# Performance work log

Hardware: AMD Instinct MI355X
Metric: run time of the kernel (lower is better)

## Reference

```python
import jax, jax.numpy as jnp
import numpy as np

EMB = 1024
HEADS = 16
HD = EMB // HEADS
EPS = 1e-5

def _ln(x, g, b):
    m = jnp.mean(x, axis=-1, keepdims=True)
    v = jnp.mean((x - m) ** 2, axis=-1, keepdims=True)
    return (x - m) * jax.lax.rsqrt(v + EPS) * g + b

def setup_inputs() -> dict:
    key = jax.random.key(0)
    ks = jax.random.split(key, 12)
    s_in = 1.0 / np.sqrt(EMB)
    s_ff = 1.0 / np.sqrt(4 * EMB)
    return {
        "x": jax.random.normal(ks[0], (2, 2048, EMB), jnp.float32),
        "wq": jax.random.uniform(ks[1], (HEADS, EMB, HD), jnp.float32, -s_in, s_in),
        "wk": jax.random.uniform(ks[2], (HEADS, EMB, HD), jnp.float32, -s_in, s_in),
        "wv": jax.random.uniform(ks[3], (HEADS, EMB, HD), jnp.float32, -s_in, s_in),
        "wo": jax.random.uniform(ks[4], (EMB, EMB), jnp.float32, -s_in, s_in),
        "bo": jax.random.uniform(ks[5], (EMB,), jnp.float32, -s_in, s_in),
        "g1": jnp.ones((EMB,), jnp.float32),
        "b1": jnp.zeros((EMB,), jnp.float32),
        "g2": jnp.ones((EMB,), jnp.float32),
        "b2": jnp.zeros((EMB,), jnp.float32),
        "w1": jax.random.uniform(ks[6], (EMB, 4 * EMB), jnp.float32, -s_in, s_in),
        "bf1": jax.random.uniform(ks[7], (4 * EMB,), jnp.float32, -s_in, s_in),
        "w2": jax.random.uniform(ks[8], (4 * EMB, EMB), jnp.float32, -s_ff, s_ff),
        "bf2": jax.random.uniform(ks[9], (EMB,), jnp.float32, -s_ff, s_ff),
    }

def reference(x, wq, wk, wv, wo, bo, g1, b1, g2, b2, w1, bf1, w2, bf2):
    B, T, C = x.shape
    h = _ln(x, g1, b1)
    # all heads batched: [B,H,T,HD]
    q = jnp.einsum('btc,hcd->bhtd', h, wq)
    k = jnp.einsum('btc,hcd->bhtd', h, wk)
    v = jnp.einsum('btc,hcd->bhtd', h, wv)
    # NOTE: original scales by full emb_size C**-0.5, not head_size
    scores = jnp.einsum('bhtd,bhsd->bhts', q, k) * (C ** -0.5)
    causal = jnp.tril(jnp.ones((T, T), bool))
    scores = jnp.where(causal, scores, -jnp.inf)
    w = jax.nn.softmax(scores, axis=-1)
    attn = jnp.einsum('bhts,bhsd->bhtd', w, v)
    attn = attn.transpose(0, 2, 1, 3).reshape(B, T, C)  # concat heads
    x = x + attn @ wo + bo
    h2 = _ln(x, g2, b2)
    ffn = jax.nn.relu(h2 @ w1 + bf1) @ w2 + bf2
    return x + ffn
```

## Files before the change

### kernel.cpp

```cpp
#include <hip/hip_runtime.h>
#include <hip/hip_bf16.h>

typedef __bf16 bf16x8 __attribute__((ext_vector_type(8)));
typedef float f32x4 __attribute__((ext_vector_type(4)));
typedef short s16x8 __attribute__((ext_vector_type(8)));

#define DEV __device__ __forceinline__

DEV float b2f(unsigned short u) {
  unsigned int x = ((unsigned int)u) << 16;
  return __builtin_bit_cast(float, x);
}
DEV unsigned short f2b(float f) {
  unsigned int x = __builtin_bit_cast(unsigned int, f);
  x += 0x7fffu + ((x >> 16) & 1u);
  return (unsigned short)(x >> 16);
}
DEV unsigned int f2b2(float a, float b) {
  float2 t; t.x = a; t.y = b;
  __hip_bfloat162 v = __float22bfloat162_rn(t);
  unsigned int r;
  __builtin_memcpy(&r, &v, 4);
  return r;
}
DEV f32x4 mfma16(bf16x8 a, bf16x8 b, f32x4 c) {
  return __builtin_amdgcn_mfma_f32_16x16x32_bf16(a, b, c, 0, 0, 0);
}
DEV void gl2lds16(const unsigned short* g, unsigned short* l) {
  __builtin_amdgcn_global_load_lds(
      (const __attribute__((address_space(1))) void*)g,
      (__attribute__((address_space(3))) void*)l, 16, 0, 0);
}

__global__ __launch_bounds__(256)
void transpose_k(const float* __restrict__ in, unsigned short* __restrict__ out,
                 int K, int N, long zin, long zout) {
  __shared__ float tile[32][33];
  in  += (size_t)blockIdx.z * zin;
  out += (size_t)blockIdx.z * zout;
  int n0 = blockIdx.x * 32, k0 = blockIdx.y * 32;
  int tx = threadIdx.x, ty = threadIdx.y;
  #pragma unroll
  for (int i = ty; i < 32; i += 8)
    tile[i][tx] = in[(size_t)(k0 + i) * N + n0 + tx];
  __syncthreads();
  #pragma unroll
  for (int i = ty; i < 32; i += 8)
    out[(size_t)(n0 + i) * K + k0 + tx] = f2b(tile[tx][i]);
}

__global__ __launch_bounds__(256)
void transpose_qkv(const float* __restrict__ wq, const float* __restrict__ wk,
                   const float* __restrict__ wv, unsigned short* __restrict__ out) {
  __shared__ float tile[32][33];
  const int z = blockIdx.z;
  const float* in = (z < 16) ? (wq + (size_t)z * 65536)
                  : (z < 32) ? (wk + (size_t)(z - 16) * 65536)
                             : (wv + (size_t)(z - 32) * 65536);
  unsigned short* o = out + (size_t)z * 65536;
  int n0 = blockIdx.x * 32, k0 = blockIdx.y * 32;
  int tx = threadIdx.x, ty = threadIdx.y;
  #pragma unroll
  for (int i = ty; i < 32; i += 8)
    tile[i][tx] = in[(size_t)(k0 + i) * 64 + n0 + tx];
  __syncthreads();
  #pragma unroll
  for (int i = ty; i < 32; i += 8)
    o[(size_t)(n0 + i) * 1024 + k0 + tx] = f2b(tile[tx][i]);
}

__global__ __launch_bounds__(256)
void ln_kernel(const float* __restrict__ x, const float* __restrict__ g,
               const float* __restrict__ b, unsigned short* __restrict__ o) {
  __shared__ float rs[4];
  __shared__ float rq[4];
  int row = blockIdx.x, tid = threadIdx.x;
  const float* xr = x + (size_t)row * 1024;
  float4 raw = ((const float4*)xr)[tid];
  float s = raw.x + raw.y + raw.z + raw.w;
  float q = raw.x*raw.x + raw.y*raw.y + raw.z*raw.z + raw.w*raw.w;
  #pragma unroll
  for (int off = 32; off > 0; off >>= 1) {
    s += __shfl_down(s, off);
    q += __shfl_down(q, off);
  }
  int wave = tid >> 6;
  if ((tid & 63) == 0) { rs[wave] = s; rq[wave] = q; }
  __syncthreads();
  float ts = rs[0] + rs[1] + rs[2] + rs[3];
  float tq = rq[0] + rq[1] + rq[2] + rq[3];
  float mean = ts * (1.0f/1024.0f);
  float var = tq * (1.0f/1024.0f) - mean*mean;
  float rstd = rsqrtf(var + 1e-5f);
  float4 gr = ((const float4*)g)[tid];
  float4 br = ((const float4*)b)[tid];
  float o0 = (raw.x-mean)*rstd*gr.x + br.x;
  float o1 = (raw.y-mean)*rstd*gr.y + br.y;
  float o2 = (raw.z-mean)*rstd*gr.z + br.z;
  float o3 = (raw.w-mean)*rstd*gr.w + br.w;
  uint2 ov;
  ov.x = f2b2(o0, o1);
  ov.y = f2b2(o2, o3);
  ((uint2*)(o + (size_t)row * 1024))[tid] = ov;
}

template<bool RELU, bool BIAS, bool VFUSE>
__global__ __launch_bounds__(512, 2)
void gemm8p(const unsigned short* __restrict__ A, const unsigned short* __restrict__ Bt,
            const float* __restrict__ bias, void* __restrict__ Cv,
            unsigned short* __restrict__ vT, int NTn, int N, int K) {
  __shared__ unsigned short As[4][256*32];
  __shared__ unsigned short Bs[4][256*32];
  const int tid = threadIdx.x;
  const int lane = tid & 63, wave = tid >> 6;
  const int quad = lane >> 4, l16 = lane & 15;
  const int wm = wave >> 2, wn = wave & 3;
  const int nwg = gridDim.x;
  const int id = blockIdx.x;
  const int id2 = (id & 7) * (nwg >> 3) + (id >> 3);
  const int mt = id2 / NTn, nt = id2 % NTn;
  const int m0 = mt * 256, n0 = nt * 256;

  f32x4 acc[8][4];
  #pragma unroll
  for (int i = 0; i < 8; ++i)
    #pragma unroll
    for (int j = 0; j < 4; ++j) acc[i][j] = (f32x4){0.f, 0.f, 0.f, 0.f};

  const int srow = tid >> 2;
  const int scc  = (((tid & 3) ^ ((srow >> 1) & 3)) * 8);
  const unsigned short* Ab = A + (size_t)m0 * K;
  const unsigned short* Bb = Bt + (size_t)n0 * K;

  const int NT = K >> 5;
  const int H  = NT << 2;

  auto stage = [&](int h) {
    const int Tt = h >> 2, part = h & 3, kk = Tt << 5;
    const int buf = Tt & 3;
    if (part == 0)
      gl2lds16(Ab + (size_t)srow * K + kk + scc,         &As[buf][tid * 8]);
    else if (part == 1)
      gl2lds16(Ab + (size_t)(srow + 128) * K + kk + scc, &As[buf][4096 + tid * 8]);
    else if (part == 2)
      gl2lds16(Bb + (size_t)srow * K + kk + scc,         &Bs[buf][tid * 8]);
    else
      gl2lds16(Bb + (size_t)(srow + 128) * K + kk + scc, &Bs[buf][4096 + tid * 8]);
  };

  #pragma unroll
  for (int h = 0; h < 10; ++h) stage(h);
  asm volatile("s_waitcnt vmcnt(6)" ::: "memory");
  asm volatile("s_barrier" ::: "memory");

  const int qsw = (quad ^ ((l16 >> 1) & 3)) * 8;
  const int arow0 = wm * 128 + l16;
  const int brow0 = wn * 64 + l16;

  for (int T = 0; T < NT; ++T) {
    const int buf = T & 3;
    bf16x8 bq[4];
    {
      bf16x8 af[4];
      #pragma unroll
      for (int i = 0; i < 4; ++i)
        af[i] = __builtin_bit_cast(bf16x8,
          *(const s16x8*)&As[buf][(arow0 + i*16)*32 + qsw]);
      #pragma unroll
      for (int j = 0; j < 4; ++j)
        bq[j] = __builtin_bit_cast(bf16x8,
          *(const s16x8*)&Bs[buf][(brow0 + j*16)*32 + qsw]);
      const int h = 4*T + 10;
      if (h < H)     stage(h);
      if (h + 1 < H) stage(h + 1);
      asm volatile("s_barrier" ::: "memory");
      __builtin_amdgcn_s_setprio(1);
      #pragma unroll
      for (int i = 0; i < 4; ++i)
        #pragma unroll
        for (int j = 0; j < 4; ++j)
          acc[i][j] = mfma16(af[i], bq[j], acc[i][j]);
      __builtin_amdgcn_s_setprio(0);
      asm volatile("s_barrier" ::: "memory");
    }
    {
      bf16x8 af[4];
      #pragma unroll
      for (int i = 0; i < 4; ++i)
        af[i] = __builtin_bit_cast(bf16x8,
          *(const s16x8*)&As[buf][(arow0 + 64 + i*16)*32 + qsw]);
      const int h = 4*T + 12;
      if (h < H)     stage(h);
      if (h + 1 < H) stage(h + 1);
      if (T + 3 < NT)      { asm volatile("s_waitcnt vmcnt(6)" ::: "memory"); }
      else if (T + 2 < NT) { asm volatile("s_waitcnt vmcnt(4)" ::: "memory"); }
      else if (T + 1 < NT) { asm volatile("s_waitcnt vmcnt(0)" ::: "memory"); }
      asm volatile("s_barrier" ::: "memory");
      __builtin_amdgcn_s_setprio(1);
      #pragma unroll
      for (int i = 0; i < 4; ++i)
        #pragma unroll
        for (int j = 0; j < 4; ++j)
          acc[4 + i][j] = mfma16(af[i], bq[j], acc[4 + i][j]);
      __builtin_amdgcn_s_setprio(0);
      asm volatile("s_barrier" ::: "memory");
    }
  }

  #pragma unroll
  for (int ii = 0; ii < 8; ++ii) {
    const int row = m0 + wm*128 + ii*16 + quad*4;
    #pragma unroll
    for (int j = 0; j < 4; ++j) {
      const int col = n0 + wn*64 + j*16 + l16;
      if (VFUSE && col >= 2048) {
        const int b = row >> 11, tloc = row & 2047;
        const int h = (col - 2048) >> 6, d = col & 63;
        ushort4 pk;
        pk.x = f2b(acc[ii][j][0]);
        pk.y = f2b(acc[ii][j][1]);
        pk.z = f2b(acc[ii][j][2]);
        pk.w = f2b(acc[ii][j][3]);
        *(ushort4*)&vT[((size_t)((b*16 + h)*64 + d))*2048 + tloc] = pk;
      } else {
        float bv = BIAS ? bias[col] : 0.f;
        #pragma unroll
        for (int r = 0; r < 4; ++r) {
          float v = acc[ii][j][r] + bv;
          if (RELU) v = fmaxf(v, 0.f);
          ((unsigned short*)Cv)[(size_t)(row + r) * N + col] = f2b(v);
        }
      }
    }
  }
}

__global__ __launch_bounds__(512)
void gemm_t128(const unsigned short* __restrict__ A, const unsigned short* __restrict__ Bt,
               const float* __restrict__ bias, const float* __restrict__ resid,
               float* __restrict__ C, int M, int N, int K) {
  __shared__ unsigned short SMEM[6*128*64];
  const int tid = threadIdx.x;
  const int lane = tid & 63;
  const int quad = lane >> 4, l16 = lane & 15;
  const int wave = tid >> 6;
  const int sub = wave >> 2;
  const int wq = wave & 3;
  const int wm = (wq >> 1) * 64, wn = (wq & 1) * 64;
  const int id = blockIdx.x;
  const int xcd = id & 7, i2 = id >> 3;
  const int mt = (xcd << 2) | (i2 >> 3);
  const int nt = i2 & 7;
  const int m0 = mt * 128, n0 = nt * 128;

  f32x4 acc[4][4];
  #pragma unroll
  for (int i = 0; i < 4; ++i)
    #pragma unroll
    for (int j = 0; j < 4; ++j) acc[i][j] = (f32x4){0.f, 0.f, 0.f, 0.f};

  const int srow = tid >> 3;
  const int scc  = ((tid & 7) ^ (srow & 7)) * 8;
  const unsigned short* Ab = A + (size_t)m0 * K;
  const unsigned short* Bb = Bt + (size_t)n0 * K;

  auto stage = [&](int buf, int k0) {
    unsigned short* Ad = SMEM + buf * 8192;
    unsigned short* Bd = SMEM + 24576 + buf * 8192;
    gl2lds16(Ab + (size_t)srow * K + k0 + scc,        Ad + tid * 8);
    gl2lds16(Ab + (size_t)(srow + 64) * K + k0 + scc, Ad + 4096 + tid * 8);
    gl2lds16(Bb + (size_t)srow * K + k0 + scc,        Bd + tid * 8);
    gl2lds16(Bb + (size_t)(srow + 64) * K + k0 + scc, Bd + 4096 + tid * 8);
  };

  const int niter = K >> 6;
  stage(0, 0);
  stage(1, 64);

  const int cc = sub * 4 + quad;
  int bufc = 0;
  for (int it = 0; it < niter; ++it) {
    if (it + 1 < niter) {
      asm volatile("s_waitcnt vmcnt(4)" ::: "memory");
    } else {
      asm volatile("s_waitcnt vmcnt(0)" ::: "memory");
    }
    __builtin_amdgcn_s_barrier();
    if (it + 2 < niter) {
      int bufn = bufc + 2; if (bufn >= 3) bufn -= 3;
      stage(bufn, (it + 2) * 64);
    }
    const unsigned short* Ar = SMEM + bufc * 8192;
    const unsigned short* Br = SMEM + 24576 + bufc * 8192;
    bf16x8 af[4], bfr[4];
    #pragma unroll
    for (int i = 0; i < 4; ++i) {
      const int R = wm + i*16 + l16;
      af[i] = __builtin_bit_cast(bf16x8,
        *(const s16x8*)&Ar[R*64 + ((cc ^ (R & 7)) * 8)]);
    }
    #pragma unroll
    for (int j = 0; j < 4; ++j) {
      const int R = wn + j*16 + l16;
      bfr[j] = __builtin_bit_cast(bf16x8,
        *(const s16x8*)&Br[R*64 + ((cc ^ (R & 7)) * 8)]);
    }
    #pragma unroll
    for (int i = 0; i < 4; ++i)
      #pragma unroll
      for (int j = 0; j < 4; ++j)
        acc[i][j] = mfma16(af[i], bfr[j], acc[i][j]);
    bufc = (bufc == 2) ? 0 : bufc + 1;
  }

  __syncthreads();
  float* ex = (float*)&SMEM[0];
  float* w = ex + wq * 4096;
  if (sub == 1) {
    #pragma unroll
    for (int i = 0; i < 4; ++i)
      #pragma unroll
      for (int j = 0; j < 4; ++j)
        *(f32x4*)&w[(i*4 + j)*256 + lane*4] = acc[i][j];
  }
  __syncthreads();
  if (sub == 1) return;

  #pragma unroll
  for (int i = 0; i < 4; ++i) {
    const int row = m0 + wm + i*16 + quad*4;
    #pragma unroll
    for (int j = 0; j < 4; ++j) {
      f32x4 oth = *(const f32x4*)&w[(i*4 + j)*256 + lane*4];
      const int col = n0 + wn + j*16 + l16;
      const float bv = bias[col];
      #pragma unroll
      for (int r = 0; r < 4; ++r)
        C[(size_t)(row + r) * N + col] =
            acc[i][j][r] + oth[r] + bv + resid[(size_t)(row + r) * N + col];
    }
  }
}

__global__ __launch_bounds__(256)
void attn_kernel(const unsigned short* __restrict__ qkv,
                 const unsigned short* __restrict__ vT,
                 unsigned short* __restrict__ outc) {
  __shared__ unsigned short Ks[2][64*64];
  __shared__ unsigned short Vs[2][64*64];
  __shared__ unsigned short Ps[4*16*72];
  const int tid = threadIdx.x, lane = tid & 63, wave = tid >> 6;
  const int quad = lane >> 4, l16 = lane & 15;
  const int bh = blockIdx.y, b = bh >> 4, h = bh & 15;
  const int jA = blockIdx.x, jB = 31 - jA;
  const size_t tokbase = (size_t)b * 2048 * 3072;
  const unsigned short* Q  = qkv + tokbase + h * 64;
  const unsigned short* Kg = qkv + tokbase + 1024 + h * 64;
  const unsigned short* Vg = vT + (size_t)bh * 64 * 2048;

  const s16x8 ones_s = {0x3F80, 0x3F80, 0x3F80, 0x3F80, 0x3F80, 0x3F80, 0x3F80, 0x3F80};
  const bf16x8 onesf = __builtin_bit_cast(bf16x8, ones_s);

  bf16x8 qf[2][2];
  #pragma unroll
  for (int t = 0; t < 2; ++t) {
    const int qrow = (t ? jB : jA) * 64 + wave * 16 + l16;
    #pragma unroll
    for (int s = 0; s < 2; ++s) {
      s16x8 raw = *(const s16x8*)(Q + (size_t)qrow * 3072 + s * 32 + quad * 8);
      unsigned short* rp = (unsigned short*)&raw;
      #pragma unroll
      for (int j = 0; j < 8; ++j) rp[j] = f2b(b2f(rp[j]) * 0.03125f);
      qf[t][s] = __builtin_bit_cast(bf16x8, raw);
    }
  }

  f32x4 accO[2][4];
  f32x4 accS[2] = {(f32x4){0.f,0.f,0.f,0.f}, (f32x4){0.f,0.f,0.f,0.f}};
  #pragma unroll
  for (int t = 0; t < 2; ++t)
    #pragma unroll
    for (int i = 0; i < 4; ++i) accO[t][i] = (f32x4){0.f, 0.f, 0.f, 0.f};

  const int r8 = lane >> 3;
  const int cs = (((lane & 7) ^ r8) * 8);

  auto stage = [&](int buf, int kv0) {
    #pragma unroll
    for (int i = 0; i < 2; ++i) {
      int row = wave * 16 + i * 8;
      gl2lds16(Kg + (size_t)(kv0 + row + r8) * 3072 + cs, &Ks[buf][row * 64 + lane * 8]);
      gl2lds16(Vg + (size_t)(row + r8) * 2048 + kv0 + cs, &Vs[buf][row * 64 + lane * 8]);
    }
  };

  const int ntile = jB + 1;
  stage(0, 0);
  __syncthreads();

  for (int it = 0; it < ntile; ++it) {
    const int buf = it & 1;
    if (it + 1 < ntile) stage(buf ^ 1, (it + 1) * 64);

    #pragma unroll
    for (int t = 0; t < 2; ++t) {
      const int jT = t ? jB : jA;
      if (it > jT) continue;
      f32x4 sv[4];
      #pragma unroll
      for (int ni = 0; ni < 4; ++ni) {
        sv[ni] = (f32x4){0.f, 0.f, 0.f, 0.f};
        #pragma unroll
        for (int s = 0; s < 2; ++s) {
          bf16x8 kf = __builtin_bit_cast(bf16x8,
            *(const s16x8*)&Ks[buf][(ni*16 + l16)*64 + (((s*4 + quad) ^ (l16 & 7)) * 8)]);
          sv[ni] = mfma16(qf[t][s], kf, sv[ni]);
        }
      }
      if (it == jT) {
        const int rowg = jT*64 + wave*16 + quad*4;
        const int kv0 = it * 64;
        #pragma unroll
        for (int ni = 0; ni < 4; ++ni) {
          const int colg = kv0 + ni*16 + l16;
          #pragma unroll
          for (int r = 0; r < 4; ++r)
            if (colg > rowg + r) sv[ni][r] = -__builtin_inff();
        }
      }
      #pragma unroll
      for (int ni = 0; ni < 4; ++ni) {
        float p0 = __expf(sv[ni][0]);
        float p1 = __expf(sv[ni][1]);
        float p2 = __expf(sv[ni][2]);
        float p3 = __expf(sv[ni][3]);
        unsigned int u01 = f2b2(p0, p1);
        unsigned int u23 = f2b2(p2, p3);
        const int base = wave*1152 + ni*16 + l16;
        Ps[base + (quad*4 + 0)*72] = (unsigned short)u01;
        Ps[base + (quad*4 + 1)*72] = (unsigned short)(u01 >> 16);
        Ps[base + (quad*4 + 2)*72] = (unsigned short)u23;
        Ps[base + (quad*4 + 3)*72] = (unsigned short)(u23 >> 16);
      }
      __asm__ volatile("s_waitcnt lgkmcnt(0)" ::: "memory");
      #pragma unroll
      for (int s = 0; s < 2; ++s) {
        bf16x8 pf = __builtin_bit_cast(bf16x8,
          *(const s16x8*)&Ps[wave*1152 + l16*72 + s*32 + quad*8]);
        accS[t] = mfma16(pf, onesf, accS[t]);
        #pragma unroll
        for (int ni = 0; ni < 4; ++ni) {
          bf16x8 vf = __builtin_bit_cast(bf16x8,
            *(const s16x8*)&Vs[buf][(ni*16 + l16)*64 + (((s*4 + quad) ^ (l16 & 7)) * 8)]);
          accO[t][ni] = mfma16(pf, vf, accO[t][ni]);
        }
      }
    }
    __syncthreads();
  }

  #pragma unroll
  for (int t = 0; t < 2; ++t) {
    const int rowg = (t ? jB : jA)*64 + wave*16 + quad*4;
    float inv[4];
    #pragma unroll
    for (int r = 0; r < 4; ++r) inv[r] = __builtin_amdgcn_rcpf(accS[t][r]);
    #pragma unroll
    for (int ni = 0; ni < 4; ++ni)
      #pragma unroll
      for (int r = 0; r < 4; ++r)
        outc[(size_t)(b*2048 + rowg + r) * 1024 + h*64 + ni*16 + l16]
          = f2b(accO[t][ni][r] * inv[r]);
  }
}

extern "C" void kernel_launch(void* const* d_in, const int* in_sizes, int n_in,
                              void* d_out, int out_size, void* d_ws, size_t ws_size,
                              hipStream_t stream) {
  (void)in_sizes; (void)n_in; (void)out_size; (void)ws_size;
  const float* x   = (const float*)d_in[0];
  const float* wq  = (const float*)d_in[1];
  const float* wk  = (const float*)d_in[2];
  const float* wv  = (const float*)d_in[3];
  const float* wo  = (const float*)d_in[4];
  const float* bo  = (const float*)d_in[5];
  const float* g1  = (const float*)d_in[6];
  const float* b1  = (const float*)d_in[7];
  const float* g2  = (const float*)d_in[8];
  const float* b2  = (const float*)d_in[9];
  const float* w1  = (const float*)d_in[10];
  const float* bf1 = (const float*)d_in[11];
  const float* w2  = (const float*)d_in[12];
  const float* bf2 = (const float*)d_in[13];
  float* out = (float*)d_out;

  unsigned short* ws    = (unsigned short*)d_ws;
  unsigned short* wqkvt = ws;
  unsigned short* wot   = wqkvt + 3*1024*1024;
  unsigned short* w1t   = wot   + 1024*1024;
  unsigned short* w2t   = w1t   + 4096*1024;
  unsigned short* hbuf  = w2t   + 4096*1024;
  unsigned short* qkvb  = hbuf  + 4096*1024;
  unsigned short* attnb = qkvb  + (size_t)4096*3072;
  float*          x2b   = (float*)(attnb + 4096*1024);
  unsigned short* vTb   = (unsigned short*)x2b;
  unsigned short* midb  = qkvb;

  dim3 tb(32, 8);
  transpose_qkv<<<dim3(2,32,48), tb, 0, stream>>>(wq, wk, wv, wqkvt);
  transpose_k<<<dim3(32,32,1),  tb, 0, stream>>>(wo, wot, 1024, 1024, 0, 0);
  transpose_k<<<dim3(128,32,1), tb, 0, stream>>>(w1, w1t, 1024, 4096, 0, 0);
  transpose_k<<<dim3(32,128,1), tb, 0, stream>>>(w2, w2t, 4096, 1024, 0, 0);

  ln_kernel<<<4096, 256, 0, stream>>>(x, g1, b1, hbuf);
  gemm8p<false,false,true><<<192, 512, 0, stream>>>(
      hbuf, wqkvt, nullptr, qkvb, vTb, 12, 3072, 1024);
  attn_kernel<<<dim3(16,32), 256, 0, stream>>>(qkvb, vTb, attnb);
  gemm_t128<<<256, 512, 0, stream>>>(attnb, wot, bo, x, x2b, 4096, 1024, 1024);
  ln_kernel<<<4096, 256, 0, stream>>>(x2b, g2, b2, hbuf);
  gemm8p<true,true,false><<<256, 512, 0, stream>>>(
      hbuf, w1t, bf1, midb, nullptr, 16, 4096, 1024);
  gemm_t128<<<256, 512, 0, stream>>>(midb, w2t, bf2, x2b, out, 4096, 1024, 4096);
}
```

Before: 325.8 us.

## Split paired causal attention blocks into one query tile per block with XCD-aware mapping

Each attention block previously handled two query tiles (j and 31-j) so causal work was balanced per block and shared K/V staging. Now each block handles a single 64-row query tile, doubling the grid to 1024 blocks, and the 1D block id is remapped so that all blocks for a given batch-head land on the same XCD, improving L2 reuse of K/V. This trades away the built-in load balance and the shared K/V loads for more parallelism and cache locality, so blocks now have very uneven work (1 to 32 tiles).

```diff
diff --git a/kernel.cpp b/kernel.cpp
--- a/kernel.cpp
+++ b/kernel.cpp
@@ -351,8 +351,12 @@
   __shared__ unsigned short Ps[4*16*72];
   const int tid = threadIdx.x, lane = tid & 63, wave = tid >> 6;
   const int quad = lane >> 4, l16 = lane & 15;
-  const int bh = blockIdx.y, b = bh >> 4, h = bh & 15;
-  const int jA = blockIdx.x, jB = 31 - jA;
+  const int id = blockIdx.x;
+  const int xcd = id & 7;
+  const int w = id >> 3;
+  const int bh = xcd * 4 + (w & 3);
+  const int j = w >> 2;
+  const int b = bh >> 4, h = bh & 15;
   const size_t tokbase = (size_t)b * 2048 * 3072;
   const unsigned short* Q  = qkv + tokbase + h * 64;
   const unsigned short* Kg = qkv + tokbase + 1024 + h * 64;
@@ -361,26 +365,23 @@
   const s16x8 ones_s = {0x3F80, 0x3F80, 0x3F80, 0x3F80, 0x3F80, 0x3F80, 0x3F80, 0x3F80};
   const bf16x8 onesf = __builtin_bit_cast(bf16x8, ones_s);
 
-  bf16x8 qf[2][2];
-  #pragma unroll
-  for (int t = 0; t < 2; ++t) {
-    const int qrow = (t ? jB : jA) * 64 + wave * 16 + l16;
+  bf16x8 qf[2];
+  {
+    const int qrow = j * 64 + wave * 16 + l16;
     #pragma unroll
     for (int s = 0; s < 2; ++s) {
       s16x8 raw = *(const s16x8*)(Q + (size_t)qrow * 3072 + s * 32 + quad * 8);
       unsigned short* rp = (unsigned short*)&raw;
       #pragma unroll
-      for (int j = 0; j < 8; ++j) rp[j] = f2b(b2f(rp[j]) * 0.03125f);
-      qf[t][s] = __builtin_bit_cast(bf16x8, raw);
-    }
-  }
-
-  f32x4 accO[2][4];
-  f32x4 accS[2] = {(f32x4){0.f,0.f,0.f,0.f}, (f32x4){0.f,0.f,0.f,0.f}};
-  #pragma unroll
-  for (int t = 0; t < 2; ++t)
-    #pragma unroll
-    for (int i = 0; i < 4; ++i) accO[t][i] = (f32x4){0.f, 0.f, 0.f, 0.f};
+      for (int k = 0; k < 8; ++k) rp[k] = f2b(b2f(rp[k]) * 0.03125f);
+      qf[s] = __builtin_bit_cast(bf16x8, raw);
+    }
+  }
+
+  f32x4 accO[4];
+  f32x4 accS = (f32x4){0.f, 0.f, 0.f, 0.f};
+  #pragma unroll
+  for (int i = 0; i < 4; ++i) accO[i] = (f32x4){0.f, 0.f, 0.f, 0.f};
 
   const int r8 = lane >> 3;
   const int cs = (((lane & 7) ^ r8) * 8);
@@ -394,7 +395,7 @@
     }
   };
 
-  const int ntile = jB + 1;
+  const int ntile = j + 1;
   stage(0, 0);
   __syncthreads();
 
@@ -402,76 +403,68 @@
     const int buf = it & 1;
     if (it + 1 < ntile) stage(buf ^ 1, (it + 1) * 64);
 
-    #pragma unroll
-    for (int t = 0; t < 2; ++t) {
-      const int jT = t ? jB : jA;
-      if (it > jT) continue;
-      f32x4 sv[4];
+    f32x4 sv[4];
+    #pragma unroll
+    for (int ni = 0; ni < 4; ++ni) {
+      sv[ni] = (f32x4){0.f, 0.f, 0.f, 0.f};
+      #pragma unroll
+      for (int s = 0; s < 2; ++s) {
+        bf16x8 kf = __builtin_bit_cast(bf16x8,
+          *(const s16x8*)&Ks[buf][(ni*16 + l16)*64 + (((s*4 + quad) ^ (l16 & 7)) * 8)]);
+        sv[ni] = mfma16(qf[s], kf, sv[ni]);
+      }
+    }
+    if (it == j) {
+      const int rowg = j*64 + wave*16 + quad*4;
+      const int kv0 = it * 64;
       #pragma unroll
       for (int ni = 0; ni < 4; ++ni) {
-        sv[ni] = (f32x4){0.f, 0.f, 0.f, 0.f};
+        const int colg = kv0 + ni*16 + l16;
         #pragma unroll
-        for (int s = 0; s < 2; ++s) {
-          bf16x8 kf = __builtin_bit_cast(bf16x8,
-            *(const s16x8*)&Ks[buf][(ni*16 + l16)*64 + (((s*4 + quad) ^ (l16 & 7)) * 8)]);
-          sv[ni] = mfma16(qf[t][s], kf, sv[ni]);
-        }
+        for (int r = 0; r < 4; ++r)
+          if (colg > rowg + r) sv[ni][r] = -__builtin_inff();
       }
-      if (it == jT) {
-        const int rowg = jT*64 + wave*16 + quad*4;
-        const int kv0 = it * 64;
-        #pragma unroll
-        for (int ni = 0; ni < 4; ++ni) {
-          const int colg = kv0 + ni*16 + l16;
-          #pragma unroll
-          for (int r = 0; r < 4; ++r)
-            if (colg > rowg + r) sv[ni][r] = -__builtin_inff();
-        }
+    }
+    #pragma unroll
+    for (int ni = 0; ni < 4; ++ni) {
+      float p0 = __expf(sv[ni][0]);
+      float p1 = __expf(sv[ni][1]);
+      float p2 = __expf(sv[ni][2]);
+      float p3 = __expf(sv[ni][3]);
+      unsigned int u01 = f2b2(p0, p1);
+      unsigned int u23 = f2b2(p2, p3);
+      const int base = wave*1152 + ni*16 + l16;
+      Ps[base + (quad*4 + 0)*72] = (unsigned short)u01;
+      Ps[base + (quad*4 + 1)*72] = (unsigned short)(u01 >> 16);
+      Ps[base + (quad*4 + 2)*72] = (unsigned short)u23;
+      Ps[base + (quad*4 + 3)*72] = (unsigned short)(u23 >> 16);
+    }
+    __asm__ volatile("s_waitcnt lgkmcnt(0)" ::: "memory");
+    #pragma unroll
+    for (int s = 0; s < 2; ++s) {
+      bf16x8 pf = __builtin_bit_cast(bf16x8,
+        *(const s16x8*)&Ps[wave*1152 + l16*72 + s*32 + quad*8]);
+      accS = mfma16(pf, onesf, accS);
+      #pragma unroll
+      for (int ni = 0; ni < 4; ++ni) {
+        bf16x8 vf = __builtin_bit_cast(bf16x8,
+          *(const s16x8*)&Vs[buf][(ni*16 + l16)*64 + (((s*4 + quad) ^ (l16 & 7)) * 8)]);
+        accO[ni] = mfma16(pf, vf, accO[ni]);
       }
-      #pragma unroll
-      for (int ni = 0; ni < 4; ++ni) {
-        float p0 = __expf(sv[ni][0]);
-        float p1 = __expf(sv[ni][1]);
-        float p2 = __expf(sv[ni][2]);
-        float p3 = __expf(sv[ni][3]);
-        unsigned int u01 = f2b2(p0, p1);
-        unsigned int u23 = f2b2(p2, p3);
-        const int base = wave*1152 + ni*16 + l16;
-        Ps[base + (quad*4 + 0)*72] = (unsigned short)u01;
-        Ps[base + (quad*4 + 1)*72] = (unsigned short)(u01 >> 16);
-        Ps[base + (quad*4 + 2)*72] = (unsigned short)u23;
-        Ps[base + (quad*4 + 3)*72] = (unsigned short)(u23 >> 16);
-      }
-      __asm__ volatile("s_waitcnt lgkmcnt(0)" ::: "memory");
-      #pragma unroll
-      for (int s = 0; s < 2; ++s) {
-        bf16x8 pf = __builtin_bit_cast(bf16x8,
-          *(const s16x8*)&Ps[wave*1152 + l16*72 + s*32 + quad*8]);
-        accS[t] = mfma16(pf, onesf, accS[t]);
-        #pragma unroll
-        for (int ni = 0; ni < 4; ++ni) {
-          bf16x8 vf = __builtin_bit_cast(bf16x8,
-            *(const s16x8*)&Vs[buf][(ni*16 + l16)*64 + (((s*4 + quad) ^ (l16 & 7)) * 8)]);
-          accO[t][ni] = mfma16(pf, vf, accO[t][ni]);
-        }
-      }
     }
     __syncthreads();
   }
 
-  #pragma unroll
-  for (int t = 0; t < 2; ++t) {
-    const int rowg = (t ? jB : jA)*64 + wave*16 + quad*4;
-    float inv[4];
-    #pragma unroll
-    for (int r = 0; r < 4; ++r) inv[r] = __builtin_amdgcn_rcpf(accS[t][r]);
-    #pragma unroll
-    for (int ni = 0; ni < 4; ++ni)
-      #pragma unroll
-      for (int r = 0; r < 4; ++r)
-        outc[(size_t)(b*2048 + rowg + r) * 1024 + h*64 + ni*16 + l16]
-          = f2b(accO[t][ni][r] * inv[r]);
-  }
+  const int rowg = j*64 + wave*16 + quad*4;
+  float inv[4];
+  #pragma unroll
+  for (int r = 0; r < 4; ++r) inv[r] = __builtin_amdgcn_rcpf(accS[r]);
+  #pragma unroll
+  for (int ni = 0; ni < 4; ++ni)
+    #pragma unroll
+    for (int r = 0; r < 4; ++r)
+      outc[(size_t)(b*2048 + rowg + r) * 1024 + h*64 + ni*16 + l16]
+        = f2b(accO[ni][r] * inv[r]);
 }
 
 extern "C" void kernel_launch(void* const* d_in, const int* in_sizes, int n_in,
@@ -515,7 +508,7 @@
   ln_kernel<<<4096, 256, 0, stream>>>(x, g1, b1, hbuf);
   gemm8p<false,false,true><<<192, 512, 0, stream>>>(
       hbuf, wqkvt, nullptr, qkvb, vTb, 12, 3072, 1024);
-  attn_kernel<<<dim3(16,32), 256, 0, stream>>>(qkvb, vTb, attnb);
+  attn_kernel<<<1024, 256, 0, stream>>>(qkvb, vTb, attnb);
   gemm_t128<<<256, 512, 0, stream>>>(attnb, wot, bo, x, x2b, 4096, 1024, 1024);
   ln_kernel<<<4096, 256, 0, stream>>>(x2b, g2, b2, hbuf);
   gemm8p<true,true,false><<<256, 512, 0, stream>>>(
```

After: 325.9 us. Within noise of the previous version (+0.0%).

## Transpose score MFMA for vectorized P stores, use exp2, and remap attention blocks per XCD

Applied to the files above, without the earlier changes.

The attention kernel now computes S^T by swapping the MFMA operands, so each lane holds four consecutive kv scores for one query row. That lets the bf16 probabilities go to shared memory as a single 8-byte store instead of four scattered 2-byte stores. The softmax scale is folded with log2(e) so exp2f replaces __expf. The grid is flattened to 1D and remapped so the four heads sharing an XCD (id&7) reuse K/V in that XCD's L2. The causal mask indexing is rewritten to match the transposed layout, and the remapping assumes round-robin dispatch of blocks across the 8 XCDs.

```diff
diff --git a/kernel.cpp b/kernel.cpp
--- a/kernel.cpp
+++ b/kernel.cpp
@@ -351,8 +351,11 @@
   __shared__ unsigned short Ps[4*16*72];
   const int tid = threadIdx.x, lane = tid & 63, wave = tid >> 6;
   const int quad = lane >> 4, l16 = lane & 15;
-  const int bh = blockIdx.y, b = bh >> 4, h = bh & 15;
-  const int jA = blockIdx.x, jB = 31 - jA;
+  const int id = blockIdx.x;
+  const int xcd = id & 7;
+  const int bh = xcd * 4 + ((id >> 3) & 3);
+  const int jA = id >> 5, jB = 31 - jA;
+  const int b = bh >> 4, h = bh & 15;
   const size_t tokbase = (size_t)b * 2048 * 3072;
   const unsigned short* Q  = qkv + tokbase + h * 64;
   const unsigned short* Kg = qkv + tokbase + 1024 + h * 64;
@@ -370,7 +373,7 @@
       s16x8 raw = *(const s16x8*)(Q + (size_t)qrow * 3072 + s * 32 + quad * 8);
       unsigned short* rp = (unsigned short*)&raw;
       #pragma unroll
-      for (int j = 0; j < 8; ++j) rp[j] = f2b(b2f(rp[j]) * 0.03125f);
+      for (int k = 0; k < 8; ++k) rp[k] = f2b(b2f(rp[k]) * 0.0450842305f);
       qf[t][s] = __builtin_bit_cast(bf16x8, raw);
     }
   }
@@ -414,33 +417,29 @@
         for (int s = 0; s < 2; ++s) {
           bf16x8 kf = __builtin_bit_cast(bf16x8,
             *(const s16x8*)&Ks[buf][(ni*16 + l16)*64 + (((s*4 + quad) ^ (l16 & 7)) * 8)]);
-          sv[ni] = mfma16(qf[t][s], kf, sv[ni]);
+          sv[ni] = mfma16(kf, qf[t][s], sv[ni]);
         }
       }
       if (it == jT) {
-        const int rowg = jT*64 + wave*16 + quad*4;
-        const int kv0 = it * 64;
+        const int qr = jT*64 + wave*16 + l16;
+        const int kvb = it*64 + quad*4;
         #pragma unroll
         for (int ni = 0; ni < 4; ++ni) {
-          const int colg = kv0 + ni*16 + l16;
           #pragma unroll
           for (int r = 0; r < 4; ++r)
-            if (colg > rowg + r) sv[ni][r] = -__builtin_inff();
+            if (kvb + ni*16 + r > qr) sv[ni][r] = -__builtin_inff();
         }
       }
       #pragma unroll
       for (int ni = 0; ni < 4; ++ni) {
-        float p0 = __expf(sv[ni][0]);
-        float p1 = __expf(sv[ni][1]);
-        float p2 = __expf(sv[ni][2]);
-        float p3 = __expf(sv[ni][3]);
-        unsigned int u01 = f2b2(p0, p1);
-        unsigned int u23 = f2b2(p2, p3);
-        const int base = wave*1152 + ni*16 + l16;
-        Ps[base + (quad*4 + 0)*72] = (unsigned short)u01;
-        Ps[base + (quad*4 + 1)*72] = (unsigned short)(u01 >> 16);
-        Ps[base + (quad*4 + 2)*72] = (unsigned short)u23;
-        Ps[base + (quad*4 + 3)*72] = (unsigned short)(u23 >> 16);
+        float p0 = exp2f(sv[ni][0]);
+        float p1 = exp2f(sv[ni][1]);
+        float p2 = exp2f(sv[ni][2]);
+        float p3 = exp2f(sv[ni][3]);
+        uint2 pk2;
+        pk2.x = f2b2(p0, p1);
+        pk2.y = f2b2(p2, p3);
+        *(uint2*)&Ps[wave*1152 + l16*72 + ni*16 + quad*4] = pk2;
       }
       __asm__ volatile("s_waitcnt lgkmcnt(0)" ::: "memory");
       #pragma unroll
@@ -515,7 +514,7 @@
   ln_kernel<<<4096, 256, 0, stream>>>(x, g1, b1, hbuf);
   gemm8p<false,false,true><<<192, 512, 0, stream>>>(
       hbuf, wqkvt, nullptr, qkvb, vTb, 12, 3072, 1024);
-  attn_kernel<<<dim3(16,32), 256, 0, stream>>>(qkvb, vTb, attnb);
+  attn_kernel<<<512, 256, 0, stream>>>(qkvb, vTb, attnb);
   gemm_t128<<<256, 512, 0, stream>>>(attnb, wot, bo, x, x2b, 4096, 1024, 1024);
   ln_kernel<<<4096, 256, 0, stream>>>(x2b, g2, b2, hbuf);
   gemm8p<true,true,false><<<256, 512, 0, stream>>>(
```

Result: no change. 325.7 us (-0.0%).
